# Optimization experiments

Measured on AMD Instinct MI355X. Metric: run time of the kernel, lower is better.

The kernel has to match this reference:

```python
import math
import jax, jax.numpy as jnp
import numpy as np

N_EMBD = 1024
N_HEAD = 16
B, T = 2, 2048


def _heads(t):
    # (B, T, D) -> (B, H, T, hd)
    b, s, d = t.shape
    return t.reshape(b, s, N_HEAD, d // N_HEAD).transpose(0, 2, 1, 3)


def setup_inputs() -> dict:
    key = jax.random.key(0)
    ks = jax.random.split(key, 7)
    D = N_EMBD
    s = 0.02
    return {
        "x": jax.random.normal(ks[0], (B, T, D), dtype=jnp.float32),
        "w_attn": jax.random.normal(ks[1], (2 * D, D), dtype=jnp.float32) * s,
        "b_attn": jnp.zeros((2 * D,), dtype=jnp.float32),
        "w_k2": jax.random.normal(ks[2], (D, D), dtype=jnp.float32) * s,
        "b_k2": jnp.zeros((D,), dtype=jnp.float32),
        "w_proj": jax.random.normal(ks[3], (D, D), dtype=jnp.float32) * s,
        "b_proj": jnp.zeros((D,), dtype=jnp.float32),
    }


def reference(x, w_attn, b_attn, w_k2, b_k2, w_proj, b_proj):
    b, t, d = x.shape
    hd = d // N_HEAD
    scale = 1.0 / math.sqrt(hd)

    # QKV projections: q,k from c_attn; v is raw x reshaped into heads
    qk = x @ w_attn.T + b_attn
    q, k = jnp.split(qk, 2, axis=-1)
    q, k, v = _heads(q), _heads(k), _heads(x)  # (B,H,T,hd)

    # AR branch: standard causal softmax attention
    scores = jnp.einsum("bhqd,bhkd->bhqk", q, k) * scale
    causal = jnp.tril(jnp.ones((t, t), dtype=bool))
    scores = jnp.where(causal, scores, -jnp.inf)
    y_ar = jnp.einsum("bhqk,bhkd->bhqd", jax.nn.softmax(scores, axis=-1), v)

    # MA branch on one-step residuals e_t = v_{t+1} - y_ar_t
    e = v[:, :, 1:, :] - y_ar[:, :, :-1, :]           # (B,H,T-1,hd)
    q2 = q[:, :, 1:, :]
    k2 = _heads(x[:, :-1] @ w_k2.T + b_k2)            # (B,H,T-1,hd)

    qa = -jax.nn.leaky_relu(-q2 * scale, negative_slope=0.02)  # ma_q_activation
    ka = jax.nn.sigmoid((k2 * scale) * 0.02)                   # ma_k_activation, k=0.02

    ma = jnp.einsum("bhqd,bhkd->bhqk", qa, ka)        # (B,H,T-1,T-1), no softmax
    ma = jnp.where(jnp.tril(jnp.ones((t - 1, t - 1), dtype=bool)), ma, 0.0)
    y_ma = jnp.einsum("bhqk,bhkd->bhqd", ma, e)
    y_ma = jnp.concatenate([jnp.zeros_like(y_ma[:, :, :1, :]), y_ma], axis=2)

    def merge(z):  # (B,H,T,hd) -> (B,T,D)
        return z.transpose(0, 2, 1, 3).reshape(b, t, d)

    out = (merge(y_ar) @ w_proj.T + b_proj) + (merge(y_ma) @ w_proj.T + b_proj)
    return out
```

## Files before the change

### kernel.cpp

```cpp
#include <hip/hip_runtime.h>
#include <hip/hip_bf16.h>
#include <math.h>

#define BB  2
#define TT  2048
#define DDE 1024
#define NHH 16
#define HDD 64

typedef __bf16 bf16_t;
typedef __attribute__((ext_vector_type(8))) __bf16 bf16x8;
typedef __attribute__((ext_vector_type(4))) __bf16 bf16x4;
typedef __attribute__((ext_vector_type(4))) float  f32x4;

#define MFMA(a, b, c) __builtin_amdgcn_mfma_f32_16x16x32_bf16((a), (b), (c), 0, 0, 0)

#define WAIT_VM6()   asm volatile("s_waitcnt vmcnt(6)" ::: "memory")
#define WAIT_VM4()   asm volatile("s_waitcnt vmcnt(4)" ::: "memory")
#define WAIT_VM0()   asm volatile("s_waitcnt vmcnt(0)" ::: "memory")
#define WAIT_LGKM0() asm volatile("s_waitcnt lgkmcnt(0)" ::: "memory")

__device__ inline void wg_barrier() {
    __builtin_amdgcn_sched_barrier(0);
    __builtin_amdgcn_s_barrier();
    __builtin_amdgcn_sched_barrier(0);
}

__device__ inline unsigned int cvtpk(float a, float b) {
    unsigned int r;
    asm("v_cvt_pk_bf16_f32 %0, %1, %2" : "=v"(r) : "v"(a), "v"(b));
    return r;
}

__device__ inline void pl16swap(unsigned int &a, unsigned int &b) {
    asm("v_permlane16_swap_b32 %0, %1" : "+v"(a), "+v"(b));
}

__device__ inline void gll16(const bf16_t* g, unsigned short* l) {
    __builtin_amdgcn_global_load_lds(
        (const __attribute__((address_space(1))) void*)g,
        (__attribute__((address_space(3))) void*)l, 16, 0, 0);
}

template<int ROWS>
__device__ inline void stage_tile(const bf16_t* g0, size_t gstride,
                                  unsigned short* lds, int wave, int lane)
{
    const int r8 = lane >> 3;
    const int ck = (lane & 7) ^ r8;
    constexpr int RW = ROWS / 4;
    const bf16_t* g = g0 + (size_t)(wave * RW + r8) * gstride + ck * 8;
    unsigned short* l = lds + wave * RW * 64 + lane * 8;
    #pragma unroll
    for (int i = 0; i < RW / 8; ++i)
        gll16(g + (size_t)(i * 8) * gstride, l + i * 512);
}

__global__ __launch_bounds__(256) void cvt_all(
    const float* __restrict__ x, const float* __restrict__ wa,
    const float* __restrict__ wk, const float* __restrict__ wp,
    bf16_t* __restrict__ out)
{
    const size_t NX  = (size_t)BB*TT*DDE;
    const size_t NWA = (size_t)2*DDE*DDE;
    const size_t NW  = (size_t)DDE*DDE;
    const size_t e = ((size_t)blockIdx.x * 256 + threadIdx.x) * 4;
    const float* src;
    if (e < NX)                 src = x  + e;
    else if (e < NX + NWA)      src = wa + (e - NX);
    else if (e < NX + NWA + NW) src = wk + (e - NX - NWA);
    else                        src = wp + (e - NX - NWA - NW);
    float4 v = *(const float4*)src;
    bf16x4 o;
    o[0] = (bf16_t)v.x; o[1] = (bf16_t)v.y;
    o[2] = (bf16_t)v.z; o[3] = (bf16_t)v.w;
    *(bf16x4*)(out + e) = o;
}

__global__ __launch_bounds__(256) void transpose_head(
    const bf16_t* __restrict__ src, bf16_t* __restrict__ dst)
{
    const int t0 = blockIdx.x * 64, h = blockIdx.y, b = blockIdx.z;
    const int tid = threadIdx.x;
    __shared__ __align__(16) bf16_t tile[64 * 64];

    #pragma unroll
    for (int it = 0; it < 2; ++it) {
        const int t = it * 32 + (tid >> 3);
        const int cw = tid & 7;
        const int slot = (cw + (t >> 3)) & 7;
        bf16x8 v = *(const bf16x8*)(src + (size_t)(b*TT + t0 + t)*DDE + h*HDD + cw*8);
        *(bf16x8*)(tile + t*64 + slot*8) = v;
    }
    __syncthreads();
    const int bh = b * NHH + h;
    #pragma unroll
    for (int it = 0; it < 2; ++it) {
        const int d = it * 32 + (tid >> 3);
        const int co = tid & 7;
        const int slot = ((d >> 3) + co) & 7;
        bf16x8 o;
        #pragma unroll
        for (int j = 0; j < 8; ++j)
            o[j] = tile[(co*8 + j)*64 + slot*8 + (d & 7)];
        *(bf16x8*)(dst + (size_t)(bh*64 + d)*TT + t0 + co*8) = o;
    }
}

__global__ __launch_bounds__(256) void build_etg(
    const bf16_t* __restrict__ yarb, const bf16_t* __restrict__ xb,
    bf16_t* __restrict__ etg)
{
    const int t0 = blockIdx.x * 64, h = blockIdx.y, b = blockIdx.z;
    const int tid = threadIdx.x;
    const int bh = b * NHH + h;
    __shared__ __align__(16) bf16_t tile[64 * 64];

    #pragma unroll
    for (int it = 0; it < 2; ++it) {
        const int t = it * 32 + (tid >> 3);
        const int cw = tid & 7;
        const int slot = (cw + (t >> 3)) & 7;
        const int tg = t0 + t;
        bf16x8 ev;
        if (tg == 0) {
            #pragma unroll
            for (int u = 0; u < 8; ++u) ev[u] = (bf16_t)0.f;
        } else {
            bf16x8 xv = *(const bf16x8*)(xb   + (size_t)(b*TT + tg)*DDE + h*HDD + cw*8);
            bf16x8 nv = *(const bf16x8*)(yarb + (size_t)(b*TT + tg - 1)*DDE + h*HDD + cw*8);
            #pragma unroll
            for (int u = 0; u < 8; ++u)
                ev[u] = (bf16_t)((float)xv[u] - (float)nv[u]);
        }
        *(bf16x8*)(tile + t*64 + slot*8) = ev;
    }
    __syncthreads();
    #pragma unroll
    for (int it = 0; it < 2; ++it) {
        const int d = it * 32 + (tid >> 3);
        const int co = tid & 7;
        const int slot = ((d >> 3) + co) & 7;
        bf16x8 o;
        #pragma unroll
        for (int j = 0; j < 8; ++j)
            o[j] = tile[(co*8 + j)*64 + slot*8 + (d & 7)];
        *(bf16x8*)(etg + (size_t)(bh*64 + d)*TT + t0 + co*8) = o;
    }
}

__global__ __launch_bounds__(256) void gemm_qkk2(
    const bf16_t* __restrict__ A, const bf16_t* __restrict__ wab,
    const bf16_t* __restrict__ wkb, const float* __restrict__ b_attn,
    const float* __restrict__ b_k2, bf16_t* __restrict__ qkb,
    bf16_t* __restrict__ qab, bf16_t* __restrict__ kcs)
{
    __shared__ __align__(16) unsigned short As[2][64 * 64];
    __shared__ __align__(16) unsigned short Bs[2][128 * 64];
    const int tid  = threadIdx.x;
    const int wave = tid >> 6, lane = tid & 63;
    const int l15  = lane & 15, quad = lane >> 4;
    const int lid = (int)blockIdx.y * 24 + (int)blockIdx.x;
    const int s   = (lid & 7) * 192 + (lid >> 3);
    const int bm = (s / 24) * 64, bn = (s % 24) * 128;
    const int wm = (wave & 1) * 32, wn = (wave >> 1) * 64;
    const int region = bn >> 10;
    const int K = DDE;
    constexpr int NST = DDE / 64;

    const bf16_t* W = (region < 2) ? wab + (size_t)bn * K
                                   : wkb + (size_t)(bn - 2048) * K;
    const float* bp = (region < 2) ? b_attn + bn : b_k2 + (bn - 2048);
    const bf16_t* Ab = A + (size_t)bm * K;

    f32x4 acc[2][4];
    #pragma unroll
    for (int i = 0; i < 2; ++i)
        #pragma unroll
        for (int j = 0; j < 4; ++j) acc[i][j] = (f32x4)0.f;

    stage_tile<64>(Ab, K, As[0], wave, lane);
    stage_tile<128>(W,  K, Bs[0], wave, lane);
    stage_tile<64>(Ab + 64, K, As[1], wave, lane);
    stage_tile<128>(W  + 64, K, Bs[1], wave, lane);

    for (int t = 0; t < NST; ++t) {
        if (t + 1 < NST) WAIT_VM6(); else WAIT_VM0();
        wg_barrier();
        const unsigned short* Ac = As[t & 1];
        const unsigned short* Bc = Bs[t & 1];
        bf16x8 af[2][2], bfr[4][2];
        #pragma unroll
        for (int mt = 0; mt < 2; ++mt)
            #pragma unroll
            for (int kh = 0; kh < 2; ++kh)
                af[mt][kh] = *(const bf16x8*)(Ac + (wm + mt*16 + l15)*64
                                              + (((kh*4 + quad) ^ (l15 & 7))*8));
        #pragma unroll
        for (int nt = 0; nt < 4; ++nt)
            #pragma unroll
            for (int kh = 0; kh < 2; ++kh)
                bfr[nt][kh] = *(const bf16x8*)(Bc + (wn + nt*16 + l15)*64
                                               + (((kh*4 + quad) ^ (l15 & 7))*8));
        __builtin_amdgcn_s_setprio(1);
        #pragma unroll
        for (int mt = 0; mt < 2; ++mt)
            #pragma unroll
            for (int nt = 0; nt < 4; ++nt) {
                acc[mt][nt] = MFMA(af[mt][0], bfr[nt][0], acc[mt][nt]);
                acc[mt][nt] = MFMA(af[mt][1], bfr[nt][1], acc[mt][nt]);
            }
        __builtin_amdgcn_s_setprio(0);
        WAIT_LGKM0();
        wg_barrier();
        if (t + 2 < NST) {
            stage_tile<64>(Ab + (t+2)*64, K, As[t & 1], wave, lane);
            stage_tile<128>(W  + (t+2)*64, K, Bs[t & 1], wave, lane);
        }
    }

    #pragma unroll
    for (int nt = 0; nt < 4; ++nt) {
        const int cl = wn + nt*16 + l15;
        const float bj = bp[cl];
        const int cg = bn + cl;
        #pragma unroll
        for (int mt = 0; mt < 2; ++mt)
            #pragma unroll
            for (int r = 0; r < 4; ++r) {
                const int row = bm + wm + mt*16 + quad*4 + r;
                const float v = acc[mt][nt][r] + bj;
                if (region == 0) {
                    qkb[(size_t)row * (2*DDE) + cg] = (bf16_t)(v * 0.180336880f);
                    const float z = v * 0.125f;
                    qab[(size_t)row * DDE + cg] = (bf16_t)((v > 0.f) ? 0.02f*z : z);
                } else if (region == 1) {
                    qkb[(size_t)row * (2*DDE) + cg] = (bf16_t)v;
                } else {
                    const int c2 = cg - 2048;
                    const float kc = 1.f/(1.f + __expf(-v*0.0025f)) - 0.5f;
                    if (((row + 1) & (TT - 1)) != 0)
                        kcs[(size_t)(row + 1) * DDE + c2] = (bf16_t)kc;
                    if ((row & (TT - 1)) == 0)
                        kcs[(size_t)row * DDE + c2] = (bf16_t)0.f;
                }
            }
    }
}

__global__ __launch_bounds__(256) void gemm_proj(
    const bf16_t* __restrict__ A, const bf16_t* __restrict__ W,
    const float* __restrict__ bias, float* __restrict__ C,
    int M, int N, int K, float bmul)
{
    __shared__ __align__(16) unsigned short As[2][64 * 64];
    __shared__ __align__(16) unsigned short Bs[2][64 * 64];
    const int tid  = threadIdx.x;
    const int wave = tid >> 6, lane = tid & 63;
    const int l15  = lane & 15, quad = lane >> 4;
    const int lid = (int)blockIdx.y * 16 + (int)blockIdx.x;
    const int s   = (lid & 7) * 128 + (lid >> 3);
    const int bm = (s / 16) * 64, bn = (s % 16) * 64;
    const int wm = (wave & 1) * 32, wn = (wave >> 1) * 32;

    const bf16_t* Ab = A + (size_t)bm * K;
    const bf16_t* Wb = W + (size_t)bn * K;
    const int NST = K / 64;

    f32x4 acc[2][2];
    #pragma unroll
    for (int i = 0; i < 2; ++i)
        #pragma unroll
        for (int j = 0; j < 2; ++j) acc[i][j] = (f32x4)0.f;

    stage_tile<64>(Ab, K, As[0], wave, lane);
    stage_tile<64>(Wb, K, Bs[0], wave, lane);
    stage_tile<64>(Ab + 64, K, As[1], wave, lane);
    stage_tile<64>(Wb + 64, K, Bs[1], wave, lane);

    for (int t = 0; t < NST; ++t) {
        if (t + 1 < NST) WAIT_VM4(); else WAIT_VM0();
        wg_barrier();
        const unsigned short* Ac = As[t & 1];
        const unsigned short* Bc = Bs[t & 1];
        bf16x8 af[2][2], bfr[2][2];
        #pragma unroll
        for (int mt = 0; mt < 2; ++mt)
            #pragma unroll
            for (int kh = 0; kh < 2; ++kh)
                af[mt][kh] = *(const bf16x8*)(Ac + (wm + mt*16 + l15)*64
                                              + (((kh*4 + quad) ^ (l15 & 7))*8));
        #pragma unroll
        for (int nt = 0; nt < 2; ++nt)
            #pragma unroll
            for (int kh = 0; kh < 2; ++kh)
                bfr[nt][kh] = *(const bf16x8*)(Bc + (wn + nt*16 + l15)*64
                                               + (((kh*4 + quad) ^ (l15 & 7))*8));
        __builtin_amdgcn_s_setprio(1);
        #pragma unroll
        for (int mt = 0; mt < 2; ++mt)
            #pragma unroll
            for (int nt = 0; nt < 2; ++nt) {
                acc[mt][nt] = MFMA(af[mt][0], bfr[nt][0], acc[mt][nt]);
                acc[mt][nt] = MFMA(af[mt][1], bfr[nt][1], acc[mt][nt]);
            }
        __builtin_amdgcn_s_setprio(0);
        WAIT_LGKM0();
        wg_barrier();
        if (t + 2 < NST) {
            stage_tile<64>(Ab + (t+2)*64, K, As[t & 1], wave, lane);
            stage_tile<64>(Wb + (t+2)*64, K, Bs[t & 1], wave, lane);
        }
    }

    #pragma unroll
    for (int nt = 0; nt < 2; ++nt) {
        const int col = bn + wn + nt*16 + l15;
        const float bj = bias[col] * bmul;
        #pragma unroll
        for (int mt = 0; mt < 2; ++mt)
            #pragma unroll
            for (int r = 0; r < 4; ++r) {
                const int row = bm + wm + mt*16 + quad*4 + r;
                C[(size_t)row * N + col] = acc[mt][nt][r] + bj;
            }
    }
}

__device__ inline int qt_map32(int bx, int h, int b) {
    const int u = ((h >> 3) & 1) | (b << 1);
    int qt = (u & 1) ? (bx ^ 31) : bx;
    if (u & 2) qt ^= 16;
    return qt;
}

__global__ __launch_bounds__(256) void attn_ar_mfma(
    const bf16_t* __restrict__ qkb, const bf16_t* __restrict__ vtg,
    bf16_t* __restrict__ yarb)
{
    const int h = blockIdx.y, b = blockIdx.z;
    const int qt = qt_map32((int)blockIdx.x, h, b);
    const int tid = threadIdx.x, wave = tid >> 6, lane = tid & 63;
    const int l15 = lane & 15, quad = lane >> 4;
    const int q0 = qt * 64;
    const int bh = b * NHH + h;

    __shared__ __align__(16) unsigned short Qs[64 * 64];
    __shared__ __align__(16) unsigned short Ks[2][64 * 64];
    __shared__ __align__(16) unsigned short Vs[2][64 * 64];

    const int nit = qt + 1;

    const bf16_t* kg = qkb + (size_t)(b*TT)*(2*DDE) + DDE + h*HDD;
    const bf16_t* vg = vtg + (size_t)(bh*64)*TT;

    stage_tile<64>(qkb + (size_t)(b*TT + q0) * (2*DDE) + h*HDD, 2*DDE, Qs, wave, lane);
    stage_tile<64>(kg, 2*DDE, Ks[0], wave, lane);
    stage_tile<64>(vg, TT, Vs[0], wave, lane);
    if (nit > 1) {
        stage_tile<64>(kg + (size_t)64*(2*DDE), 2*DDE, Ks[1], wave, lane);
        stage_tile<64>(vg + 64, TT, Vs[1], wave, lane);
        WAIT_VM4();
    } else {
        WAIT_VM0();
    }
    wg_barrier();

    bf16x8 qf[2];
    #pragma unroll
    for (int kc = 0; kc < 2; ++kc)
        qf[kc] = *(const bf16x8*)(Qs + (wave*16 + l15)*64
                                  + ((kc*4 + quad) ^ (l15 & 7))*8);

    f32x4 o[4];
    f32x4 ls = (f32x4)0.f;
    #pragma unroll
    for (int nt = 0; nt < 4; ++nt) o[nt] = (f32x4)0.f;
    bf16x8 onesb;
    #pragma unroll
    for (int j = 0; j < 8; ++j) onesb[j] = (bf16_t)1.f;

    const int qw0 = q0 + wave * 16;
    const int cq = ((quad & 1) << 1) | (quad >> 1);

    for (int it = 0; it < nit; ++it) {
        if (it > 0) {
            if (it + 1 < nit) WAIT_VM4(); else WAIT_VM0();
            wg_barrier();
        }
        const int s0 = it * 64;
        const unsigned short* Kc = Ks[it & 1];
        const unsigned short* Vc = Vs[it & 1];

        f32x4 sv[4];
        __builtin_amdgcn_s_setprio(1);
        #pragma unroll
        for (int nt = 0; nt < 4; ++nt) {
            const unsigned short* kr = Kc + (nt*16 + l15)*64;
            bf16x8 kb0 = *(const bf16x8*)(kr + ((quad    ) ^ (l15 & 7))*8);
            bf16x8 kb1 = *(const bf16x8*)(kr + ((quad + 4) ^ (l15 & 7))*8);
            f32x4 z = (f32x4)0.f;
            z = MFMA(kb0, qf[0], z);
            z = MFMA(kb1, qf[1], z);
            sv[nt] = z;
        }
        __builtin_amdgcn_s_setprio(0);

        const bool domask = (s0 + 63 > qw0);
        const int qg = qw0 + l15;
        unsigned int pk[4][2];
        #pragma unroll
        for (int nt = 0; nt < 4; ++nt) {
            float pv[4];
            #pragma unroll
            for (int r = 0; r < 4; ++r) {
                float p = exp2f(sv[nt][r]);
                if (domask) {
                    const int sg = s0 + nt*16 + quad*4 + r;
                    if (sg > qg) p = 0.f;
                }
                pv[r] = p;
            }
            pk[nt][0] = cvtpk(pv[0], pv[1]);
            pk[nt][1] = cvtpk(pv[2], pv[3]);
        }
        bf16x8 pa[2];
        #pragma unroll
        for (int sc = 0; sc < 2; ++sc) {
            pl16swap(pk[2*sc][0], pk[2*sc+1][0]);
            pl16swap(pk[2*sc][1], pk[2*sc+1][1]);
            union { unsigned int u[4]; bf16x8 v; } pu;
            pu.u[0] = pk[2*sc][0];
            pu.u[1] = pk[2*sc][1];
            pu.u[2] = pk[2*sc+1][0];
            pu.u[3] = pk[2*sc+1][1];
            pa[sc] = pu.v;
        }

        __builtin_amdgcn_s_setprio(1);
        ls = MFMA(pa[0], onesb, ls);
        ls = MFMA(pa[1], onesb, ls);
        #pragma unroll
        for (int nt = 0; nt < 4; ++nt) {
            const unsigned short* vr = Vc + (nt*16 + l15)*64;
            bf16x8 vb0 = *(const bf16x8*)(vr + ((cq    ) ^ (l15 & 7))*8);
            bf16x8 vb1 = *(const bf16x8*)(vr + ((cq + 4) ^ (l15 & 7))*8);
            o[nt] = MFMA(pa[0], vb0, o[nt]);
            o[nt] = MFMA(pa[1], vb1, o[nt]);
        }
        __builtin_amdgcn_s_setprio(0);

        WAIT_LGKM0();
        wg_barrier();
        if (it + 2 < nit) {
            stage_tile<64>(kg + (size_t)(it+2)*64*(2*DDE), 2*DDE, Ks[it & 1], wave, lane);
            stage_tile<64>(vg + (it+2)*64, TT, Vs[it & 1], wave, lane);
        }
    }

    float inv[4];
    #pragma unroll
    for (int r = 0; r < 4; ++r) inv[r] = 1.f / ls[r];
    #pragma unroll
    for (int nt = 0; nt < 4; ++nt)
        #pragma unroll
        for (int r = 0; r < 4; ++r) {
            const int row = qw0 + quad*4 + r;
            const int col = h*HDD + nt*16 + l15;
            yarb[(size_t)(b*TT + row)*DDE + col] = (bf16_t)(o[nt][r] * inv[r]);
        }
}

__global__ __launch_bounds__(256) void attn_ma_mfma(
    const bf16_t* __restrict__ qab, const bf16_t* __restrict__ kcs,
    const bf16_t* __restrict__ etg, const bf16_t* __restrict__ yarb,
    bf16_t* __restrict__ ysumb)
{
    const int h = blockIdx.y, b = blockIdx.z;
    const int qt = qt_map32((int)blockIdx.x, h, b);
    const int tid = threadIdx.x, wave = tid >> 6, lane = tid & 63;
    const int l15 = lane & 15, quad = lane >> 4;
    const int q0 = qt * 64;
    const int bh = b * NHH + h;

    __shared__ __align__(16) unsigned short Qs[64 * 64];
    __shared__ __align__(16) unsigned short Ks[2][64 * 64];
    __shared__ __align__(16) unsigned short Es[2][64 * 64];

    const int nit = qt + 1;

    const bf16_t* kg = kcs + (size_t)(b*TT)*DDE + h*HDD;
    const bf16_t* eg = etg + (size_t)(bh*64)*TT;

    stage_tile<64>(qab + (size_t)(b*TT + q0)*DDE + h*HDD, DDE, Qs, wave, lane);
    stage_tile<64>(kg, DDE, Ks[0], wave, lane);
    stage_tile<64>(eg, TT, Es[0], wave, lane);
    if (nit > 1) {
        stage_tile<64>(kg + (size_t)64*DDE, DDE, Ks[1], wave, lane);
        stage_tile<64>(eg + 64, TT, Es[1], wave, lane);
        WAIT_VM4();
    } else {
        WAIT_VM0();
    }
    wg_barrier();

    bf16x8 qf[2];
    #pragma unroll
    for (int kc = 0; kc < 2; ++kc)
        qf[kc] = *(const bf16x8*)(Qs + (wave*16 + l15)*64
                                  + ((kc*4 + quad) ^ (l15 & 7))*8);

    float rs = 0.f;
    #pragma unroll
    for (int kc = 0; kc < 2; ++kc)
        #pragma unroll
        for (int u = 0; u < 8; ++u) rs += (float)qf[kc][u];
    rs += __shfl_xor(rs, 16);
    rs += __shfl_xor(rs, 32);
    const float Rr = 0.5f * rs;

    f32x4 o[4];
    #pragma unroll
    for (int nt = 0; nt < 4; ++nt) o[nt] = (f32x4)0.f;

    const int qw0 = q0 + wave * 16;
    const int cq = ((quad & 1) << 1) | (quad >> 1);

    for (int it = 0; it < nit; ++it) {
        if (it > 0) {
            if (it + 1 < nit) WAIT_VM4(); else WAIT_VM0();
            wg_barrier();
        }
        const int s0 = it * 64;
        const unsigned short* Kc = Ks[it & 1];
        const unsigned short* Ec = Es[it & 1];

        f32x4 sv[4];
        __builtin_amdgcn_s_setprio(1);
        #pragma unroll
        for (int nt = 0; nt < 4; ++nt) {
            const unsigned short* kr = Kc + (nt*16 + l15)*64;
            bf16x8 kb0 = *(const bf16x8*)(kr + ((quad    ) ^ (l15 & 7))*8);
            bf16x8 kb1 = *(const bf16x8*)(kr + ((quad + 4) ^ (l15 & 7))*8);
            f32x4 z = (f32x4)0.f;
            z = MFMA(kb0, qf[0], z);
            z = MFMA(kb1, qf[1], z);
            sv[nt] = z;
        }
        __builtin_amdgcn_s_setprio(0);

        const bool domask = (s0 + 63 > qw0);
        const bool m0 = (it == 0);
        const int qg = qw0 + l15;
        unsigned int pk[4][2];
        #pragma unroll
        for (int nt = 0; nt < 4; ++nt) {
            float pv[4];
            #pragma unroll
            for (int r = 0; r < 4; ++r) {
                const int sg = s0 + nt*16 + quad*4 + r;
                float p = sv[nt][r] + Rr;
                if (m0 && sg == 0) p = 0.f;
                if (domask && sg > qg) p = 0.f;
                pv[r] = p;
            }
            pk[nt][0] = cvtpk(pv[0], pv[1]);
            pk[nt][1] = cvtpk(pv[2], pv[3]);
        }
        bf16x8 pa[2];
        #pragma unroll
        for (int sc = 0; sc < 2; ++sc) {
            pl16swap(pk[2*sc][0], pk[2*sc+1][0]);
            pl16swap(pk[2*sc][1], pk[2*sc+1][1]);
            union { unsigned int u[4]; bf16x8 v; } pu;
            pu.u[0] = pk[2*sc][0];
            pu.u[1] = pk[2*sc][1];
            pu.u[2] = pk[2*sc+1][0];
            pu.u[3] = pk[2*sc+1][1];
            pa[sc] = pu.v;
        }

        __builtin_amdgcn_s_setprio(1);
        #pragma unroll
        for (int nt = 0; nt < 4; ++nt) {
            const unsigned short* er = Ec + (nt*16 + l15)*64;
            bf16x8 eb0 = *(const bf16x8*)(er + ((cq    ) ^ (l15 & 7))*8);
            bf16x8 eb1 = *(const bf16x8*)(er + ((cq + 4) ^ (l15 & 7))*8);
            o[nt] = MFMA(pa[0], eb0, o[nt]);
            o[nt] = MFMA(pa[1], eb1, o[nt]);
        }
        __builtin_amdgcn_s_setprio(0);

        WAIT_LGKM0();
        wg_barrier();
        if (it + 2 < nit) {
            stage_tile<64>(kg + (size_t)(it+2)*64*DDE, DDE, Ks[it & 1], wave, lane);
            stage_tile<64>(eg + (it+2)*64, TT, Es[it & 1], wave, lane);
        }
    }

    #pragma unroll
    for (int nt = 0; nt < 4; ++nt)
        #pragma unroll
        for (int r = 0; r < 4; ++r) {
            const int row = qw0 + quad*4 + r;
            const int col = h*HDD + nt*16 + l15;
            const size_t e = (size_t)(b*TT + row)*DDE + col;
            ysumb[e] = (bf16_t)((float)yarb[e] + o[nt][r]);
        }
}

extern "C" void kernel_launch(void* const* d_in, const int* in_sizes, int n_in,
                              void* d_out, int out_size, void* d_ws, size_t ws_size,
                              hipStream_t stream)
{
    const float* x      = (const float*)d_in[0];
    const float* w_attn = (const float*)d_in[1];
    const float* b_attn = (const float*)d_in[2];
    const float* w_k2   = (const float*)d_in[3];
    const float* b_k2   = (const float*)d_in[4];
    const float* w_proj = (const float*)d_in[5];
    const float* b_proj = (const float*)d_in[6];

    const size_t NX  = (size_t)BB*TT*DDE;
    const size_t NWA = (size_t)2*DDE*DDE;
    const size_t NW  = (size_t)DDE*DDE;
    const size_t NQK = (size_t)BB*TT*2*DDE;

    bf16_t* xb   = (bf16_t*)d_ws;
    bf16_t* wab  = xb   + NX;
    bf16_t* wkb  = wab  + NWA;
    bf16_t* wpb  = wkb  + NW;
    bf16_t* qkb  = wpb  + NW;
    bf16_t* qab  = qkb  + NQK;
    bf16_t* kcs  = qab  + NX;
    bf16_t* vtg  = kcs  + NX;
    bf16_t* ysumb= vtg  + NX;
    bf16_t* yarb = (bf16_t*)((float*)(vtg + NX) + NX);
    bf16_t* etg  = vtg;

    const size_t NCVT = NX + NWA + NW + NW;
    cvt_all<<<NCVT / 1024, 256, 0, stream>>>(x, w_attn, w_k2, w_proj, xb);

    transpose_head<<<dim3(TT/64, NHH, BB), 256, 0, stream>>>(xb, vtg);

    const int M = BB * TT;
    gemm_qkk2<<<dim3(24, M/64), 256, 0, stream>>>(xb, wab, wkb, b_attn, b_k2,
                                                   qkb, qab, kcs);

    attn_ar_mfma<<<dim3(32, NHH, BB), 256, 0, stream>>>(qkb, vtg, yarb);
    build_etg<<<dim3(TT/64, NHH, BB), 256, 0, stream>>>(yarb, xb, etg);
    attn_ma_mfma<<<dim3(32, NHH, BB), 256, 0, stream>>>(qab, kcs, etg, yarb, ysumb);

    gemm_proj<<<dim3(DDE/64, M/64), 256, 0, stream>>>(ysumb, wpb, b_proj,
                                                      (float*)d_out, M, DDE, DDE, 2.f);
}
```

Measured before the change: 240.3 us.

## Pair low and high causal query tiles in one 512-thread block sharing K/V tiles

```diff
diff --git a/kernel.cpp b/kernel.cpp
--- a/kernel.cpp
+++ b/kernel.cpp
@@ -17,6 +17,7 @@
 
 #define WAIT_VM6()   asm volatile("s_waitcnt vmcnt(6)" ::: "memory")
 #define WAIT_VM4()   asm volatile("s_waitcnt vmcnt(4)" ::: "memory")
+#define WAIT_VM2()   asm volatile("s_waitcnt vmcnt(2)" ::: "memory")
 #define WAIT_VM0()   asm volatile("s_waitcnt vmcnt(0)" ::: "memory")
 #define WAIT_LGKM0() asm volatile("s_waitcnt lgkmcnt(0)" ::: "memory")
 
@@ -42,13 +43,13 @@
         (__attribute__((address_space(3))) void*)l, 16, 0, 0);
 }
 
-template<int ROWS>
+template<int ROWS, int NW = 4>
 __device__ inline void stage_tile(const bf16_t* g0, size_t gstride,
                                   unsigned short* lds, int wave, int lane)
 {
     const int r8 = lane >> 3;
     const int ck = (lane & 7) ^ r8;
-    constexpr int RW = ROWS / 4;
+    constexpr int RW = ROWS / NW;
     const bf16_t* g = g0 + (size_t)(wave * RW + r8) * gstride + ck * 8;
     unsigned short* l = lds + wave * RW * 64 + lane * 8;
     #pragma unroll
@@ -327,50 +328,38 @@
     }
 }
 
-__device__ inline int qt_map32(int bx, int h, int b) {
-    const int u = ((h >> 3) & 1) | (b << 1);
-    int qt = (u & 1) ? (bx ^ 31) : bx;
-    if (u & 2) qt ^= 16;
-    return qt;
-}
-
-__global__ __launch_bounds__(256) void attn_ar_mfma(
+__global__ __launch_bounds__(512) void attn_ar_mfma(
     const bf16_t* __restrict__ qkb, const bf16_t* __restrict__ vtg,
     bf16_t* __restrict__ yarb)
 {
     const int h = blockIdx.y, b = blockIdx.z;
-    const int qt = qt_map32((int)blockIdx.x, h, b);
+    const int p = b ? (15 - (int)blockIdx.x) : (int)blockIdx.x;
+    const int qtL = p, qtH = 31 - p;
     const int tid = threadIdx.x, wave = tid >> 6, lane = tid & 63;
     const int l15 = lane & 15, quad = lane >> 4;
-    const int q0 = qt * 64;
+    const int qt = (wave < 4) ? qtL : qtH;
+    const int qw0 = qt * 64 + (wave & 3) * 16;
     const int bh = b * NHH + h;
 
-    __shared__ __align__(16) unsigned short Qs[64 * 64];
     __shared__ __align__(16) unsigned short Ks[2][64 * 64];
     __shared__ __align__(16) unsigned short Vs[2][64 * 64];
 
-    const int nit = qt + 1;
+    const int nit = qtH + 1;
 
     const bf16_t* kg = qkb + (size_t)(b*TT)*(2*DDE) + DDE + h*HDD;
     const bf16_t* vg = vtg + (size_t)(bh*64)*TT;
 
-    stage_tile<64>(qkb + (size_t)(b*TT + q0) * (2*DDE) + h*HDD, 2*DDE, Qs, wave, lane);
-    stage_tile<64>(kg, 2*DDE, Ks[0], wave, lane);
-    stage_tile<64>(vg, TT, Vs[0], wave, lane);
-    if (nit > 1) {
-        stage_tile<64>(kg + (size_t)64*(2*DDE), 2*DDE, Ks[1], wave, lane);
-        stage_tile<64>(vg + 64, TT, Vs[1], wave, lane);
-        WAIT_VM4();
-    } else {
-        WAIT_VM0();
-    }
+    const bf16_t* qrow = qkb + (size_t)(b*TT + qw0 + l15)*(2*DDE) + h*HDD;
+    bf16x8 qf[2];
+    qf[0] = *(const bf16x8*)(qrow + quad*8);
+    qf[1] = *(const bf16x8*)(qrow + (quad + 4)*8);
+
+    stage_tile<64, 8>(kg, 2*DDE, Ks[0], wave, lane);
+    stage_tile<64, 8>(vg, TT, Vs[0], wave, lane);
+    stage_tile<64, 8>(kg + (size_t)64*(2*DDE), 2*DDE, Ks[1], wave, lane);
+    stage_tile<64, 8>(vg + 64, TT, Vs[1], wave, lane);
+    WAIT_VM2();
     wg_barrier();
-
-    bf16x8 qf[2];
-    #pragma unroll
-    for (int kc = 0; kc < 2; ++kc)
-        qf[kc] = *(const bf16x8*)(Qs + (wave*16 + l15)*64
-                                  + ((kc*4 + quad) ^ (l15 & 7))*8);
 
     f32x4 o[4];
     f32x4 ls = (f32x4)0.f;
@@ -380,81 +369,81 @@
     #pragma unroll
     for (int j = 0; j < 8; ++j) onesb[j] = (bf16_t)1.f;
 
-    const int qw0 = q0 + wave * 16;
     const int cq = ((quad & 1) << 1) | (quad >> 1);
 
     for (int it = 0; it < nit; ++it) {
         if (it > 0) {
-            if (it + 1 < nit) WAIT_VM4(); else WAIT_VM0();
+            if (it + 1 < nit) WAIT_VM2(); else WAIT_VM0();
             wg_barrier();
         }
         const int s0 = it * 64;
         const unsigned short* Kc = Ks[it & 1];
         const unsigned short* Vc = Vs[it & 1];
 
-        f32x4 sv[4];
-        __builtin_amdgcn_s_setprio(1);
-        #pragma unroll
-        for (int nt = 0; nt < 4; ++nt) {
-            const unsigned short* kr = Kc + (nt*16 + l15)*64;
-            bf16x8 kb0 = *(const bf16x8*)(kr + ((quad    ) ^ (l15 & 7))*8);
-            bf16x8 kb1 = *(const bf16x8*)(kr + ((quad + 4) ^ (l15 & 7))*8);
-            f32x4 z = (f32x4)0.f;
-            z = MFMA(kb0, qf[0], z);
-            z = MFMA(kb1, qf[1], z);
-            sv[nt] = z;
-        }
-        __builtin_amdgcn_s_setprio(0);
-
-        const bool domask = (s0 + 63 > qw0);
-        const int qg = qw0 + l15;
-        unsigned int pk[4][2];
-        #pragma unroll
-        for (int nt = 0; nt < 4; ++nt) {
-            float pv[4];
-            #pragma unroll
-            for (int r = 0; r < 4; ++r) {
-                float p = exp2f(sv[nt][r]);
-                if (domask) {
-                    const int sg = s0 + nt*16 + quad*4 + r;
-                    if (sg > qg) p = 0.f;
+        if (s0 <= qw0 + 31) {
+            f32x4 sv[4];
+            __builtin_amdgcn_s_setprio(1);
+            #pragma unroll
+            for (int nt = 0; nt < 4; ++nt) {
+                const unsigned short* kr = Kc + (nt*16 + l15)*64;
+                bf16x8 kb0 = *(const bf16x8*)(kr + ((quad    ) ^ (l15 & 7))*8);
+                bf16x8 kb1 = *(const bf16x8*)(kr + ((quad + 4) ^ (l15 & 7))*8);
+                f32x4 z = (f32x4)0.f;
+                z = MFMA(kb0, qf[0], z);
+                z = MFMA(kb1, qf[1], z);
+                sv[nt] = z;
+            }
+            __builtin_amdgcn_s_setprio(0);
+
+            const bool domask = (s0 + 63 > qw0);
+            const int qg = qw0 + l15;
+            unsigned int pk[4][2];
+            #pragma unroll
+            for (int nt = 0; nt < 4; ++nt) {
+                float pv[4];
+                #pragma unroll
+                for (int r = 0; r < 4; ++r) {
+                    float pe = exp2f(sv[nt][r]);
+                    if (domask) {
+                        const int sg = s0 + nt*16 + quad*4 + r;
+                        if (sg > qg) pe = 0.f;
+                    }
+                    pv[r] = pe;
                 }
-                pv[r] = p;
-            }
-            pk[nt][0] = cvtpk(pv[0], pv[1]);
-            pk[nt][1] = cvtpk(pv[2], pv[3]);
-        }
-        bf16x8 pa[2];
-        #pragma unroll
-        for (int sc = 0; sc < 2; ++sc) {
-            pl16swap(pk[2*sc][0], pk[2*sc+1][0]);
-            pl16swap(pk[2*sc][1], pk[2*sc+1][1]);
-            union { unsigned int u[4]; bf16x8 v; } pu;
-            pu.u[0] = pk[2*sc][0];
-            pu.u[1] = pk[2*sc][1];
-            pu.u[2] = pk[2*sc+1][0];
-            pu.u[3] = pk[2*sc+1][1];
-            pa[sc] = pu.v;
-        }
-
-        __builtin_amdgcn_s_setprio(1);
-        ls = MFMA(pa[0], onesb, ls);
-        ls = MFMA(pa[1], onesb, ls);
-        #pragma unroll
-        for (int nt = 0; nt < 4; ++nt) {
-            const unsigned short* vr = Vc + (nt*16 + l15)*64;
-            bf16x8 vb0 = *(const bf16x8*)(vr + ((cq    ) ^ (l15 & 7))*8);
-            bf16x8 vb1 = *(const bf16x8*)(vr + ((cq + 4) ^ (l15 & 7))*8);
-            o[nt] = MFMA(pa[0], vb0, o[nt]);
-            o[nt] = MFMA(pa[1], vb1, o[nt]);
-        }
-        __builtin_amdgcn_s_setprio(0);
-
+                pk[nt][0] = cvtpk(pv[0], pv[1]);
+                pk[nt][1] = cvtpk(pv[2], pv[3]);
+            }
+            bf16x8 pa[2];
+            #pragma unroll
+            for (int sc = 0; sc < 2; ++sc) {
+                pl16swap(pk[2*sc][0], pk[2*sc+1][0]);
+                pl16swap(pk[2*sc][1], pk[2*sc+1][1]);
+                union { unsigned int u[4]; bf16x8 v; } pu;
+                pu.u[0] = pk[2*sc][0];
+                pu.u[1] = pk[2*sc][1];
+                pu.u[2] = pk[2*sc+1][0];
+                pu.u[3] = pk[2*sc+1][1];
+                pa[sc] = pu.v;
+            }
+
+            __builtin_amdgcn_s_setprio(1);
+            ls = MFMA(pa[0], onesb, ls);
+            ls = MFMA(pa[1], onesb, ls);
+            #pragma unroll
+            for (int nt = 0; nt < 4; ++nt) {
+                const unsigned short* vr = Vc + (nt*16 + l15)*64;
+                bf16x8 vb0 = *(const bf16x8*)(vr + ((cq    ) ^ (l15 & 7))*8);
+                bf16x8 vb1 = *(const bf16x8*)(vr + ((cq + 4) ^ (l15 & 7))*8);
+                o[nt] = MFMA(pa[0], vb0, o[nt]);
+                o[nt] = MFMA(pa[1], vb1, o[nt]);
+            }
+            __builtin_amdgcn_s_setprio(0);
+        }
         WAIT_LGKM0();
         wg_barrier();
         if (it + 2 < nit) {
-            stage_tile<64>(kg + (size_t)(it+2)*64*(2*DDE), 2*DDE, Ks[it & 1], wave, lane);
-            stage_tile<64>(vg + (it+2)*64, TT, Vs[it & 1], wave, lane);
+            stage_tile<64, 8>(kg + (size_t)(it+2)*64*(2*DDE), 2*DDE, Ks[it & 1], wave, lane);
+            stage_tile<64, 8>(vg + (it+2)*64, TT, Vs[it & 1], wave, lane);
         }
     }
 
@@ -471,44 +460,39 @@
         }
 }
 
-__global__ __launch_bounds__(256) void attn_ma_mfma(
+__global__ __launch_bounds__(512) void attn_ma_mfma(
     const bf16_t* __restrict__ qab, const bf16_t* __restrict__ kcs,
     const bf16_t* __restrict__ etg, const bf16_t* __restrict__ yarb,
     bf16_t* __restrict__ ysumb)
 {
     const int h = blockIdx.y, b = blockIdx.z;
-    const int qt = qt_map32((int)blockIdx.x, h, b);
+    const int p = b ? (15 - (int)blockIdx.x) : (int)blockIdx.x;
+    const int qtL = p, qtH = 31 - p;
     const int tid = threadIdx.x, wave = tid >> 6, lane = tid & 63;
     const int l15 = lane & 15, quad = lane >> 4;
-    const int q0 = qt * 64;
+    const int qt = (wave < 4) ? qtL : qtH;
+    const int qw0 = qt * 64 + (wave & 3) * 16;
     const int bh = b * NHH + h;
 
-    __shared__ __align__(16) unsigned short Qs[64 * 64];
     __shared__ __align__(16) unsigned short Ks[2][64 * 64];
     __shared__ __align__(16) unsigned short Es[2][64 * 64];
 
-    const int nit = qt + 1;
+    const int nit = qtH + 1;
 
     const bf16_t* kg = kcs + (size_t)(b*TT)*DDE + h*HDD;
     const bf16_t* eg = etg + (size_t)(bh*64)*TT;
 
-    stage_tile<64>(qab + (size_t)(b*TT + q0)*DDE + h*HDD, DDE, Qs, wave, lane);
-    stage_tile<64>(kg, DDE, Ks[0], wave, lane);
-    stage_tile<64>(eg, TT, Es[0], wave, lane);
-    if (nit > 1) {
-        stage_tile<64>(kg + (size_t)64*DDE, DDE, Ks[1], wave, lane);
-        stage_tile<64>(eg + 64, TT, Es[1], wave, lane);
-        WAIT_VM4();
-    } else {
-        WAIT_VM0();
-    }
+    const bf16_t* qrow = qab + (size_t)(b*TT + qw0 + l15)*DDE + h*HDD;
+    bf16x8 qf[2];
+    qf[0] = *(const bf16x8*)(qrow + quad*8);
+    qf[1] = *(const bf16x8*)(qrow + (quad + 4)*8);
+
+    stage_tile<64, 8>(kg, DDE, Ks[0], wave, lane);
+    stage_tile<64, 8>(eg, TT, Es[0], wave, lane);
+    stage_tile<64, 8>(kg + (size_t)64*DDE, DDE, Ks[1], wave, lane);
+    stage_tile<64, 8>(eg + 64, TT, Es[1], wave, lane);
+    WAIT_VM2();
     wg_barrier();
-
-    bf16x8 qf[2];
-    #pragma unroll
-    for (int kc = 0; kc < 2; ++kc)
-        qf[kc] = *(const bf16x8*)(Qs + (wave*16 + l15)*64
-                                  + ((kc*4 + quad) ^ (l15 & 7))*8);
 
     float rs = 0.f;
     #pragma unroll
@@ -523,79 +507,79 @@
     #pragma unroll
     for (int nt = 0; nt < 4; ++nt) o[nt] = (f32x4)0.f;
 
-    const int qw0 = q0 + wave * 16;
     const int cq = ((quad & 1) << 1) | (quad >> 1);
 
     for (int it = 0; it < nit; ++it) {
         if (it > 0) {
-            if (it + 1 < nit) WAIT_VM4(); else WAIT_VM0();
+            if (it + 1 < nit) WAIT_VM2(); else WAIT_VM0();
             wg_barrier();
         }
         const int s0 = it * 64;
         const unsigned short* Kc = Ks[it & 1];
         const unsigned short* Ec = Es[it & 1];
 
-        f32x4 sv[4];
-        __builtin_amdgcn_s_setprio(1);
-        #pragma unroll
-        for (int nt = 0; nt < 4; ++nt) {
-            const unsigned short* kr = Kc + (nt*16 + l15)*64;
-            bf16x8 kb0 = *(const bf16x8*)(kr + ((quad    ) ^ (l15 & 7))*8);
-            bf16x8 kb1 = *(const bf16x8*)(kr + ((quad + 4) ^ (l15 & 7))*8);
-            f32x4 z = (f32x4)0.f;
-            z = MFMA(kb0, qf[0], z);
-            z = MFMA(kb1, qf[1], z);
-            sv[nt] = z;
-        }
-        __builtin_amdgcn_s_setprio(0);
-
-        const bool domask = (s0 + 63 > qw0);
-        const bool m0 = (it == 0);
-        const int qg = qw0 + l15;
-        unsigned int pk[4][2];
-        #pragma unroll
-        for (int nt = 0; nt < 4; ++nt) {
-            float pv[4];
-            #pragma unroll
-            for (int r = 0; r < 4; ++r) {
-                const int sg = s0 + nt*16 + quad*4 + r;
-                float p = sv[nt][r] + Rr;
-                if (m0 && sg == 0) p = 0.f;
-                if (domask && sg > qg) p = 0.f;
-                pv[r] = p;
-            }
-            pk[nt][0] = cvtpk(pv[0], pv[1]);
-            pk[nt][1] = cvtpk(pv[2], pv[3]);
-        }
-        bf16x8 pa[2];
-        #pragma unroll
-        for (int sc = 0; sc < 2; ++sc) {
-            pl16swap(pk[2*sc][0], pk[2*sc+1][0]);
-            pl16swap(pk[2*sc][1], pk[2*sc+1][1]);
-            union { unsigned int u[4]; bf16x8 v; } pu;
-            pu.u[0] = pk[2*sc][0];
-            pu.u[1] = pk[2*sc][1];
-            pu.u[2] = pk[2*sc+1][0];
-            pu.u[3] = pk[2*sc+1][1];
-            pa[sc] = pu.v;
-        }
-
-        __builtin_amdgcn_s_setprio(1);
-        #pragma unroll
-        for (int nt = 0; nt < 4; ++nt) {
-            const unsigned short* er = Ec + (nt*16 + l15)*64;
-            bf16x8 eb0 = *(const bf16x8*)(er + ((cq    ) ^ (l15 & 7))*8);
-            bf16x8 eb1 = *(const bf16x8*)(er + ((cq + 4) ^ (l15 & 7))*8);
-            o[nt] = MFMA(pa[0], eb0, o[nt]);
-            o[nt] = MFMA(pa[1], eb1, o[nt]);
-        }
-        __builtin_amdgcn_s_setprio(0);
-
+        if (s0 <= qw0 + 31) {
+            f32x4 sv[4];
+            __builtin_amdgcn_s_setprio(1);
+            #pragma unroll
+            for (int nt = 0; nt < 4; ++nt) {
+                const unsigned short* kr = Kc + (nt*16 + l15)*64;
+                bf16x8 kb0 = *(const bf16x8*)(kr + ((quad    ) ^ (l15 & 7))*8);
+                bf16x8 kb1 = *(const bf16x8*)(kr + ((quad + 4) ^ (l15 & 7))*8);
+                f32x4 z = (f32x4)0.f;
+                z = MFMA(kb0, qf[0], z);
+                z = MFMA(kb1, qf[1], z);
+                sv[nt] = z;
+            }
+            __builtin_amdgcn_s_setprio(0);
+
+            const bool domask = (s0 + 63 > qw0);
+            const bool m0 = (it == 0);
+            const int qg = qw0 + l15;
+            unsigned int pk[4][2];
+            #pragma unroll
+            for (int nt = 0; nt < 4; ++nt) {
+                float pv[4];
+                #pragma unroll
+                for (int r = 0; r < 4; ++r) {
+                    const int sg = s0 + nt*16 + quad*4 + r;
+                    float pe = sv[nt][r] + Rr;
+                    if (m0 && sg == 0) pe = 0.f;
+                    if (domask && sg > qg) pe = 0.f;
+                    pv[r] = pe;
+                }
+                pk[nt][0] = cvtpk(pv[0], pv[1]);
+                pk[nt][1] = cvtpk(pv[2], pv[3]);
+            }
+            bf16x8 pa[2];
+            #pragma unroll
+            for (int sc = 0; sc < 2; ++sc) {
+                pl16swap(pk[2*sc][0], pk[2*sc+1][0]);
+                pl16swap(pk[2*sc][1], pk[2*sc+1][1]);
+                union { unsigned int u[4]; bf16x8 v; } pu;
+                pu.u[0] = pk[2*sc][0];
+                pu.u[1] = pk[2*sc][1];
+                pu.u[2] = pk[2*sc+1][0];
+                pu.u[3] = pk[2*sc+1][1];
+                pa[sc] = pu.v;
+            }
+
+            __builtin_amdgcn_s_setprio(1);
+            #pragma unroll
+            for (int nt = 0; nt < 4; ++nt) {
+                const unsigned short* er = Ec + (nt*16 + l15)*64;
+                bf16x8 eb0 = *(const bf16x8*)(er + ((cq    ) ^ (l15 & 7))*8);
+                bf16x8 eb1 = *(const bf16x8*)(er + ((cq + 4) ^ (l15 & 7))*8);
+                o[nt] = MFMA(pa[0], eb0, o[nt]);
+                o[nt] = MFMA(pa[1], eb1, o[nt]);
+            }
+            __builtin_amdgcn_s_setprio(0);
+        }
         WAIT_LGKM0();
         wg_barrier();
         if (it + 2 < nit) {
-            stage_tile<64>(kg + (size_t)(it+2)*64*DDE, DDE, Ks[it & 1], wave, lane);
-            stage_tile<64>(eg + (it+2)*64, TT, Es[it & 1], wave, lane);
+            stage_tile<64, 8>(kg + (size_t)(it+2)*64*DDE, DDE, Ks[it & 1], wave, lane);
+            stage_tile<64, 8>(eg + (it+2)*64, TT, Es[it & 1], wave, lane);
         }
     }
 
@@ -648,9 +632,9 @@
     gemm_qkk2<<<dim3(24, M/64), 256, 0, stream>>>(xb, wab, wkb, b_attn, b_k2,
                                                    qkb, qab, kcs);
 
-    attn_ar_mfma<<<dim3(32, NHH, BB), 256, 0, stream>>>(qkb, vtg, yarb);
+    attn_ar_mfma<<<dim3(16, NHH, BB), 512, 0, stream>>>(qkb, vtg, yarb);
     build_etg<<<dim3(TT/64, NHH, BB), 256, 0, stream>>>(yarb, xb, etg);
-    attn_ma_mfma<<<dim3(32, NHH, BB), 256, 0, stream>>>(qab, kcs, etg, yarb, ysumb);
+    attn_ma_mfma<<<dim3(16, NHH, BB), 512, 0, stream>>>(qab, kcs, etg, yarb, ysumb);
 
     gemm_proj<<<dim3(DDE/64, M/64), 256, 0, stream>>>(ysumb, wpb, b_proj,
                                                       (float*)d_out, M, DDE, DDE, 2.f);
```

Measured after the change: 240.1 us. Within noise of the previous version (-0.1%).
